# Kernel tuning notes

Hardware: AMD Instinct MI355X
Metric: run time of the kernel (lower is better)

Reference implementation:

```python
import jax, jax.numpy as jnp
import numpy as np

B, D_IN, N, K, L, D_OUT = 64, 1024, 50000, 32, 3, 256


def setup_inputs() -> dict:
    key = jax.random.key(0)
    k = jax.random.split(key, 7)
    x = jax.random.normal(k[0], (B, D_IN), dtype=jnp.float32)
    W0 = jax.random.normal(k[1], (N, D_IN), dtype=jnp.float32) * 0.02
    b0 = jax.random.normal(k[2], (N,), dtype=jnp.float32) * 0.02
    Wv = jax.random.normal(k[3], (L, N, K), dtype=jnp.float32) * 0.1
    Wout = jax.random.normal(k[4], (D_OUT, N), dtype=jnp.float32) * 0.02
    bout = jax.random.normal(k[5], (D_OUT,), dtype=jnp.float32) * 0.02
    src = jax.random.randint(k[6], (L, N, K), 0, N, dtype=jnp.int64)
    return {"x": x, "W0": W0, "b0": b0, "Wv": Wv, "Wout": Wout, "bout": bout, "src": src}


def reference(x, W0, b0, Wv, Wout, bout, src):
    # layer 0: dense input->sources, relu, transpose -> [N, B]
    h = jax.nn.relu(x @ W0.T + b0).T

    # each hidden layer: per-vertex gather of K source activations + 1xK matmul + relu
    def step(h_prev, layer):
        w, s = layer                      # w: [N, K], s: [N, K]
        gathered = h_prev[s]              # [N, K, B] irregular gather
        h_new = jax.nn.relu(jnp.einsum('nk,nkb->nb', w, gathered))
        return h_new, None

    h, _ = jax.lax.scan(step, h, (Wv, src))

    # last layer -> output Linear (the module's _linear_dummy)
    return h.T @ Wout.T + bout            # [B, D_OUT]
```

## Files before the change

### kernel.cpp

```cpp
#include <hip/hip_runtime.h>

#define NV 50000
#define NVP 50176
#define BDIM 64
#define DIN 1024
#define KFAN 32
#define DOUT 256
#define KSTEPS (DIN / 32)
#define XPK_N (KSTEPS * 512)
#define OPC_CHUNK 128
#define OPC_NCH (NVP / OPC_CHUNK)

typedef short bf16x8 __attribute__((ext_vector_type(8)));
typedef float f32x4 __attribute__((ext_vector_type(4)));

__device__ __forceinline__ unsigned short bf16_rtn(float f) {
  unsigned u = __float_as_uint(f);
  return (unsigned short)((u + 0x7fffu + ((u >> 16) & 1u)) >> 16);
}
__device__ __forceinline__ float bf16_to_f(unsigned short v) {
  return __uint_as_float(((unsigned)v) << 16);
}

__global__ __launch_bounds__(256) void pack_x(const float* __restrict__ x,
                                              uint4* __restrict__ xpk8) {
  int tid = blockIdx.x * 256 + threadIdx.x;
  int ks = tid >> 8;
  int g = (tid >> 6) & 3;
  int l = tid & 63;
  int b = g * 16 + (l & 15);
  int k0 = ks * 32 + (l >> 4) * 8;
  unsigned hi[8], lo[8];
#pragma unroll
  for (int j = 0; j < 8; ++j) {
    float f = x[b * DIN + k0 + j];
    unsigned u = __float_as_uint(f);
    hi[j] = u >> 16;
    float fh = __uint_as_float(u & 0xffff0000u);
    lo[j] = bf16_rtn(f - fh);
  }
  uint4 vh, vl;
  vh.x = hi[0] | (hi[1] << 16); vh.y = hi[2] | (hi[3] << 16);
  vh.z = hi[4] | (hi[5] << 16); vh.w = hi[6] | (hi[7] << 16);
  vl.x = lo[0] | (lo[1] << 16); vl.y = lo[2] | (lo[3] << 16);
  vl.z = lo[4] | (lo[5] << 16); vl.w = lo[6] | (lo[7] << 16);
  int idx = (ks * 4 + g) * 128 + l;
#pragma unroll
  for (int c = 0; c < 8; ++c) {
    xpk8[(size_t)c * XPK_N + idx] = vh;
    xpk8[(size_t)c * XPK_N + idx + 64] = vl;
  }
}

__global__ __launch_bounds__(64) void layer0_mfma(
    const float* __restrict__ W0, const float* __restrict__ b0,
    const uint4* __restrict__ xpk8, unsigned short* __restrict__ h)
{
  const int lane = threadIdx.x;
  const int n_base = blockIdx.x * 16;
  const int rq = lane >> 4;
  const int rr = lane & 15;
  const float* wp = W0 + (size_t)(n_base + rr) * DIN + rq * 8;
  const uint4* xsrc = xpk8 + (size_t)(blockIdx.x & 7) * XPK_N;

  f32x4 acc[4];
#pragma unroll
  for (int g = 0; g < 4; ++g) acc[g] = (f32x4){0.f, 0.f, 0.f, 0.f};

  float4 wpre[4][2];
  uint4 xpre[2][8];

#pragma unroll
  for (int d = 0; d < 4; ++d) {
    wpre[d][0] = *(const float4*)(wp + d * 32);
    wpre[d][1] = *(const float4*)(wp + d * 32 + 4);
  }
#pragma unroll
  for (int d = 0; d < 2; ++d)
#pragma unroll
    for (int g = 0; g < 4; ++g) {
      xpre[d][g * 2]     = xsrc[d * 512 + g * 128 + lane];
      xpre[d][g * 2 + 1] = xsrc[d * 512 + g * 128 + 64 + lane];
    }

#pragma unroll
  for (int ks = 0; ks < KSTEPS; ++ks) {
    const int sw = ks & 3;
    const int sx = ks & 1;
    float4 wv0 = wpre[sw][0];
    float4 wv1 = wpre[sw][1];
    if (ks + 4 < KSTEPS) {
      wpre[sw][0] = *(const float4*)(wp + (ks + 4) * 32);
      wpre[sw][1] = *(const float4*)(wp + (ks + 4) * 32 + 4);
    }
    bf16x8 whi, wlo;
    {
      float wf[8] = {wv0.x, wv0.y, wv0.z, wv0.w, wv1.x, wv1.y, wv1.z, wv1.w};
#pragma unroll
      for (int e = 0; e < 8; ++e) {
        unsigned u = __float_as_uint(wf[e]);
        whi[e] = (short)(u >> 16);
        float l = wf[e] - __uint_as_float(u & 0xffff0000u);
        wlo[e] = (short)bf16_rtn(l);
      }
    }
#pragma unroll
    for (int g = 0; g < 4; ++g) {
      bf16x8 xh = __builtin_bit_cast(bf16x8, xpre[sx][g * 2]);
      bf16x8 xl = __builtin_bit_cast(bf16x8, xpre[sx][g * 2 + 1]);
      acc[g] = __builtin_amdgcn_mfma_f32_16x16x32_bf16(whi, xh, acc[g], 0, 0, 0);
      acc[g] = __builtin_amdgcn_mfma_f32_16x16x32_bf16(wlo, xh, acc[g], 0, 0, 0);
      acc[g] = __builtin_amdgcn_mfma_f32_16x16x32_bf16(whi, xl, acc[g], 0, 0, 0);
    }
    if (ks + 2 < KSTEPS) {
      const int xb = (ks + 2) * 512;
#pragma unroll
      for (int g = 0; g < 4; ++g) {
        xpre[sx][g * 2]     = xsrc[xb + g * 128 + lane];
        xpre[sx][g * 2 + 1] = xsrc[xb + g * 128 + 64 + lane];
      }
    }
  }

#pragma unroll
  for (int r = 0; r < 4; ++r) {
    int n = n_base + rq * 4 + r;
    float bias = b0[n];
#pragma unroll
    for (int g = 0; g < 4; ++g) {
      float v = fmaxf(acc[g][r] + bias, 0.f);
      h[(size_t)n * BDIM + g * 16 + rr] = bf16_rtn(v);
    }
  }
}

__global__ __launch_bounds__(256) void sparse_layer(
    const unsigned short* __restrict__ hin, const float* __restrict__ wv,
    const int* __restrict__ src, unsigned short* __restrict__ hout)
{
  const int lane = threadIdx.x & 63;
  int n = blockIdx.x * 4 + (threadIdx.x >> 6);
  n = __builtin_amdgcn_readfirstlane(n);
  const float* wrow = wv + (size_t)n * KFAN;
  const int* srow = src + (size_t)n * KFAN;
  float acc = 0.f;
#pragma unroll
  for (int k = 0; k < KFAN; ++k) {
    int s = srow[k];
    float w = wrow[k];
    acc = fmaf(w, bf16_to_f(hin[(size_t)s * BDIM + lane]), acc);
  }
  hout[(size_t)n * BDIM + lane] = bf16_rtn(fmaxf(acc, 0.f));
}

__global__ __launch_bounds__(256) void transpose_h(
    const unsigned short* __restrict__ h, unsigned short* __restrict__ hT)
{
  const int lane = threadIdx.x & 63;
  const int wv = threadIdx.x >> 6;
  const int n0 = (blockIdx.x * 4 + wv) * 8;
  unsigned short v[8];
#pragma unroll
  for (int i = 0; i < 8; ++i) {
    int n = n0 + i;
    v[i] = (n < NV) ? h[(size_t)n * BDIM + lane] : (unsigned short)0;
  }
  uint4 o;
  o.x = v[0] | ((unsigned)v[1] << 16);
  o.y = v[2] | ((unsigned)v[3] << 16);
  o.z = v[4] | ((unsigned)v[5] << 16);
  o.w = v[6] | ((unsigned)v[7] << 16);
  *(uint4*)(hT + (size_t)lane * NVP + n0) = o;
}

__global__ __launch_bounds__(64) void out_partial_mfma(
    const unsigned short* __restrict__ hT, const float* __restrict__ Wout,
    float* __restrict__ part)
{
  const int lane = threadIdx.x;
  const int rq = lane >> 4;
  const int rr = lane & 15;
  const int dtile = blockIdx.x;
  const int chunk = blockIdx.y;

  f32x4 acc[4][4];
#pragma unroll
  for (int f = 0; f < 4; ++f)
#pragma unroll
    for (int g = 0; g < 4; ++g) acc[f][g] = (f32x4){0.f, 0.f, 0.f, 0.f};

#pragma unroll
  for (int ks = 0; ks < OPC_CHUNK / 32; ++ks) {
    const int n0 = chunk * OPC_CHUNK + ks * 32 + rq * 8;
    bf16x8 hb[4];
#pragma unroll
    for (int g = 0; g < 4; ++g)
      hb[g] = *(const bf16x8*)(hT + (size_t)(g * 16 + rr) * NVP + n0);
    int nb = n0 > (NV - 8) ? (NV - 8) : n0;
#pragma unroll
    for (int f = 0; f < 4; ++f) {
      const float* wp = Wout + (size_t)(dtile * 64 + f * 16 + rr) * NV + nb;
      float4 a0 = *(const float4*)(wp);
      float4 a1 = *(const float4*)(wp + 4);
      float wf[8] = {a0.x, a0.y, a0.z, a0.w, a1.x, a1.y, a1.z, a1.w};
      bf16x8 whi, wlo;
#pragma unroll
      for (int e = 0; e < 8; ++e) {
        unsigned u = __float_as_uint(wf[e]);
        whi[e] = (short)(u >> 16);
        float l = wf[e] - __uint_as_float(u & 0xffff0000u);
        wlo[e] = (short)bf16_rtn(l);
      }
#pragma unroll
      for (int g = 0; g < 4; ++g) {
        acc[f][g] = __builtin_amdgcn_mfma_f32_16x16x32_bf16(whi, hb[g], acc[f][g], 0, 0, 0);
        acc[f][g] = __builtin_amdgcn_mfma_f32_16x16x32_bf16(wlo, hb[g], acc[f][g], 0, 0, 0);
      }
    }
  }
  float* pbase = part + ((size_t)dtile * OPC_NCH + chunk) * 4096;
#pragma unroll
  for (int f = 0; f < 4; ++f)
#pragma unroll
    for (int g = 0; g < 4; ++g)
#pragma unroll
      for (int r = 0; r < 4; ++r)
        pbase[(f * 16 + rq * 4 + r) * 64 + g * 16 + rr] = acc[f][g][r];
}

__global__ __launch_bounds__(256) void out_reduce(
    const float* __restrict__ part, const float* __restrict__ bout,
    float* __restrict__ out)
{
  int tid = blockIdx.x * 256 + threadIdx.x;
  int b = tid & 63;
  int d = tid >> 6;
  int dtile = d >> 6;
  int dd = d & 63;
  float s = bout[d];
  for (int c = 0; c < OPC_NCH; ++c)
    s += part[((size_t)dtile * OPC_NCH + c) * 4096 + dd * 64 + b];
  out[(size_t)b * DOUT + d] = s;
}

extern "C" void kernel_launch(void* const* d_in, const int* in_sizes, int n_in,
                              void* d_out, int out_size, void* d_ws, size_t ws_size,
                              hipStream_t stream)
{
  const float* x    = (const float*)d_in[0];
  const float* W0   = (const float*)d_in[1];
  const float* b0   = (const float*)d_in[2];
  const float* Wv   = (const float*)d_in[3];
  const float* Wout = (const float*)d_in[4];
  const float* bout = (const float*)d_in[5];
  const int*   src  = (const int*)d_in[6];
  float* out = (float*)d_out;

  char* ws = (char*)d_ws;
  const size_t hbf = (size_t)NV * BDIM * 2;
  const size_t hTb = (size_t)NVP * BDIM * 2;
  const size_t xpkb = (size_t)8 * XPK_N * 16;
  unsigned short* hb0 = (unsigned short*)ws;
  unsigned short* hb1 = (unsigned short*)(ws + hbf);
  unsigned short* hT  = (unsigned short*)(ws + 2 * hbf);
  uint4* xpk8 = (uint4*)(ws + 2 * hbf + hTb);
  float* part = (float*)(ws + 2 * hbf + hTb + xpkb);

  pack_x<<<32, 256, 0, stream>>>(x, xpk8);
  layer0_mfma<<<NV / 16, 64, 0, stream>>>(W0, b0, xpk8, hb0);

  const size_t lstride = (size_t)NV * KFAN;
  sparse_layer<<<NV / 4, 256, 0, stream>>>(hb0, Wv, src, hb1);
  sparse_layer<<<NV / 4, 256, 0, stream>>>(hb1, Wv + lstride, src + lstride, hb0);
  sparse_layer<<<NV / 4, 256, 0, stream>>>(hb0, Wv + 2 * lstride, src + 2 * lstride, hb1);

  transpose_h<<<NVP / 32, 256, 0, stream>>>(hb1, hT);
  out_partial_mfma<<<dim3(4, OPC_NCH), 64, 0, stream>>>(hT, Wout, part);
  out_reduce<<<(BDIM * DOUT) / 256, 256, 0, stream>>>(part, bout, out);
}
```

Before: 199.2 us.

## Switch layer0 to fp16 MFMA with pre-packed fp16 weights

Adds a repack kernel that converts W0 to fp16 in an MFMA-friendly layout, and changes layer0 to use fp16 MFMA with a single weight term and hi/lo split x. This reduces MFMA count from three to two per step and removes in-loop weight conversion. The trade-off is an extra full pass over W0 on every call plus extra writes, and reduced weight precision (fp16 with no residual term).

```diff
diff --git a/kernel.cpp b/kernel.cpp
--- a/kernel.cpp
+++ b/kernel.cpp
@@ -1,4 +1,5 @@
 #include <hip/hip_runtime.h>
+#include <hip/hip_fp16.h>
 
 #define NV 50000
 #define NVP 50176
@@ -12,6 +13,7 @@
 #define OPC_NCH (NVP / OPC_CHUNK)
 
 typedef short bf16x8 __attribute__((ext_vector_type(8)));
+typedef _Float16 f16x8 __attribute__((ext_vector_type(8)));
 typedef float f32x4 __attribute__((ext_vector_type(4)));
 
 __device__ __forceinline__ unsigned short bf16_rtn(float f) {
@@ -20,6 +22,28 @@
 }
 __device__ __forceinline__ float bf16_to_f(unsigned short v) {
   return __uint_as_float(((unsigned)v) << 16);
+}
+__device__ __forceinline__ unsigned short f16_rn(float f) {
+  return __half_as_ushort(__float2half(f));
+}
+
+__global__ __launch_bounds__(256) void repack_w(const float* __restrict__ W0,
+                                                uint4* __restrict__ Wpk) {
+  const size_t F = ((size_t)blockIdx.x * 256 + threadIdx.x) * 8;
+  float4 a = *(const float4*)(W0 + F);
+  float4 b = *(const float4*)(W0 + F + 4);
+  const int row = (int)(F >> 10);
+  const int col8 = ((int)F >> 3) & 127;
+  const int ks = col8 >> 2;
+  const int rq = col8 & 3;
+  const int nblk = row >> 4;
+  const int rr = row & 15;
+  uint4 o;
+  o.x = f16_rn(a.x) | ((unsigned)f16_rn(a.y) << 16);
+  o.y = f16_rn(a.z) | ((unsigned)f16_rn(a.w) << 16);
+  o.z = f16_rn(b.x) | ((unsigned)f16_rn(b.y) << 16);
+  o.w = f16_rn(b.z) | ((unsigned)f16_rn(b.w) << 16);
+  Wpk[(size_t)(nblk * 32 + ks) * 64 + rq * 16 + rr] = o;
 }
 
 __global__ __launch_bounds__(256) void pack_x(const float* __restrict__ x,
@@ -34,10 +58,10 @@
 #pragma unroll
   for (int j = 0; j < 8; ++j) {
     float f = x[b * DIN + k0 + j];
-    unsigned u = __float_as_uint(f);
-    hi[j] = u >> 16;
-    float fh = __uint_as_float(u & 0xffff0000u);
-    lo[j] = bf16_rtn(f - fh);
+    unsigned short h = f16_rn(f);
+    hi[j] = h;
+    float fh = __half2float(__ushort_as_half(h));
+    lo[j] = f16_rn(f - fh);
   }
   uint4 vh, vl;
   vh.x = hi[0] | (hi[1] << 16); vh.y = hi[2] | (hi[3] << 16);
@@ -53,28 +77,26 @@
 }
 
 __global__ __launch_bounds__(64) void layer0_mfma(
-    const float* __restrict__ W0, const float* __restrict__ b0,
+    const uint4* __restrict__ Wpk, const float* __restrict__ b0,
     const uint4* __restrict__ xpk8, unsigned short* __restrict__ h)
 {
   const int lane = threadIdx.x;
-  const int n_base = blockIdx.x * 16;
+  const int nblk = blockIdx.x;
+  const int n_base = nblk * 16;
   const int rq = lane >> 4;
   const int rr = lane & 15;
-  const float* wp = W0 + (size_t)(n_base + rr) * DIN + rq * 8;
-  const uint4* xsrc = xpk8 + (size_t)(blockIdx.x & 7) * XPK_N;
+  const uint4* wp = Wpk + (size_t)nblk * 32 * 64 + lane;
+  const uint4* xsrc = xpk8 + (size_t)(nblk & 7) * XPK_N;
 
   f32x4 acc[4];
 #pragma unroll
   for (int g = 0; g < 4; ++g) acc[g] = (f32x4){0.f, 0.f, 0.f, 0.f};
 
-  float4 wpre[4][2];
+  uint4 wpre[4];
   uint4 xpre[2][8];
 
 #pragma unroll
-  for (int d = 0; d < 4; ++d) {
-    wpre[d][0] = *(const float4*)(wp + d * 32);
-    wpre[d][1] = *(const float4*)(wp + d * 32 + 4);
-  }
+  for (int d = 0; d < 4; ++d) wpre[d] = wp[d * 64];
 #pragma unroll
   for (int d = 0; d < 2; ++d)
 #pragma unroll
@@ -87,30 +109,15 @@
   for (int ks = 0; ks < KSTEPS; ++ks) {
     const int sw = ks & 3;
     const int sx = ks & 1;
-    float4 wv0 = wpre[sw][0];
-    float4 wv1 = wpre[sw][1];
-    if (ks + 4 < KSTEPS) {
-      wpre[sw][0] = *(const float4*)(wp + (ks + 4) * 32);
-      wpre[sw][1] = *(const float4*)(wp + (ks + 4) * 32 + 4);
-    }
-    bf16x8 whi, wlo;
-    {
-      float wf[8] = {wv0.x, wv0.y, wv0.z, wv0.w, wv1.x, wv1.y, wv1.z, wv1.w};
-#pragma unroll
-      for (int e = 0; e < 8; ++e) {
-        unsigned u = __float_as_uint(wf[e]);
-        whi[e] = (short)(u >> 16);
-        float l = wf[e] - __uint_as_float(u & 0xffff0000u);
-        wlo[e] = (short)bf16_rtn(l);
-      }
-    }
+    uint4 wv = wpre[sw];
+    if (ks + 4 < KSTEPS) wpre[sw] = wp[(ks + 4) * 64];
+    f16x8 wf = __builtin_bit_cast(f16x8, wv);
 #pragma unroll
     for (int g = 0; g < 4; ++g) {
-      bf16x8 xh = __builtin_bit_cast(bf16x8, xpre[sx][g * 2]);
-      bf16x8 xl = __builtin_bit_cast(bf16x8, xpre[sx][g * 2 + 1]);
-      acc[g] = __builtin_amdgcn_mfma_f32_16x16x32_bf16(whi, xh, acc[g], 0, 0, 0);
-      acc[g] = __builtin_amdgcn_mfma_f32_16x16x32_bf16(wlo, xh, acc[g], 0, 0, 0);
-      acc[g] = __builtin_amdgcn_mfma_f32_16x16x32_bf16(whi, xl, acc[g], 0, 0, 0);
+      f16x8 xh = __builtin_bit_cast(f16x8, xpre[sx][g * 2]);
+      f16x8 xl = __builtin_bit_cast(f16x8, xpre[sx][g * 2 + 1]);
+      acc[g] = __builtin_amdgcn_mfma_f32_16x16x32_f16(wf, xh, acc[g], 0, 0, 0);
+      acc[g] = __builtin_amdgcn_mfma_f32_16x16x32_f16(wf, xl, acc[g], 0, 0, 0);
     }
     if (ks + 2 < KSTEPS) {
       const int xb = (ks + 2) * 512;
@@ -260,14 +267,17 @@
   const size_t hbf = (size_t)NV * BDIM * 2;
   const size_t hTb = (size_t)NVP * BDIM * 2;
   const size_t xpkb = (size_t)8 * XPK_N * 16;
+  const size_t partb = (size_t)4 * OPC_NCH * 4096 * 4;
   unsigned short* hb0 = (unsigned short*)ws;
   unsigned short* hb1 = (unsigned short*)(ws + hbf);
   unsigned short* hT  = (unsigned short*)(ws + 2 * hbf);
   uint4* xpk8 = (uint4*)(ws + 2 * hbf + hTb);
   float* part = (float*)(ws + 2 * hbf + hTb + xpkb);
+  uint4* Wpk  = (uint4*)(ws + 2 * hbf + hTb + xpkb + partb);
 
   pack_x<<<32, 256, 0, stream>>>(x, xpk8);
-  layer0_mfma<<<NV / 16, 64, 0, stream>>>(W0, b0, xpk8, hb0);
+  repack_w<<<(NV * DIN / 8) / 256, 256, 0, stream>>>(W0, Wpk);
+  layer0_mfma<<<NV / 16, 64, 0, stream>>>(Wpk, b0, xpk8, hb0);
 
   const size_t lstride = (size_t)NV * KFAN;
   sparse_layer<<<NV / 4, 256, 0, stream>>>(hb0, Wv, src, hb1);
```

After: 250.5 us. +25.7%, slower.
